# Kernel tuning notes

Measured on AMD Instinct MI355X. Metric: run time of the kernel, lower is better.

The kernel has to match this reference:

```python
import jax, jax.numpy as jnp
import numpy as np

LAMBDA_CHAMFER = 1.0
LAMBDA_EDGE = 0.1


def setup_inputs() -> dict:
    key = jax.random.key(0)
    k1, k2, k3 = jax.random.split(key, 3)
    B, N, M, E = 8, 4096, 4096, 12288
    pred_vertices = jax.random.normal(k1, (B, N, 3), dtype=jnp.float32)
    gt_vertices = jax.random.normal(k2, (B, M, 3), dtype=jnp.float32)
    edges = jax.random.randint(k3, (E, 2), 0, N, dtype=jnp.int64)
    return {"pred_vertices": pred_vertices, "gt_vertices": gt_vertices, "edges": edges}


def _pairwise_dist(p1, p2):
    # ||x - y|| computed via the expanded form to avoid a [B,N,M,3] intermediate.
    # dist2[b,n,m] = |p1[b,n]|^2 + |p2[b,m]|^2 - 2 * p1[b,n] . p2[b,m]
    sq1 = jnp.sum(p1 * p1, axis=-1)  # [B, N]
    sq2 = jnp.sum(p2 * p2, axis=-1)  # [B, M]
    cross = jnp.einsum('bnd,bmd->bnm', p1, p2)  # [B, N, M]
    dist2 = sq1[:, :, None] + sq2[:, None, :] - 2.0 * cross
    return jnp.sqrt(jnp.maximum(dist2, 0.0))


def chamfer_distance(p1, p2):
    dist = _pairwise_dist(p1, p2)  # [B, N, M]
    min_p1 = jnp.min(dist, axis=2)  # [B, N] nearest gt for each pred point
    min_p2 = jnp.min(dist, axis=1)  # [B, M] nearest pred for each gt point
    return jnp.mean(min_p1) + jnp.mean(min_p2)


def edge_length_regularization(vertices, edges):
    v1 = vertices[:, edges[:, 0]]  # [B, E, 3]
    v2 = vertices[:, edges[:, 1]]  # [B, E, 3]
    lengths = jnp.linalg.norm(v1 - v2, axis=2)  # [B, E]
    return jnp.var(lengths, ddof=1)  # torch.var is unbiased by default


def reference(pred_vertices, gt_vertices, edges):
    cd = chamfer_distance(pred_vertices, gt_vertices)
    edge_loss = edge_length_regularization(pred_vertices, edges)
    return LAMBDA_CHAMFER * cd + LAMBDA_EDGE * edge_loss
```

## Files before the change

kernel.cpp:

```cpp
#include <hip/hip_runtime.h>
#include <hip/hip_bf16.h>
#include <float.h>

constexpr int B = 8, N = 4096, M = 4096, E = 12288;
constexpr int TB = 512;
constexpr int EDGE_BLOCKS = (B * E) / TB;
constexpr int QB = 256;
constexpr int CHAM_BLOCKS = 2 * B * (N / QB);
constexpr int SPLIT = 32;
constexpr int RPT = M / SPLIT;
constexpr int VEC = 16;
constexpr int SEGSTRIDE = RPT + 1;
constexpr int REDSTRIDE = QB + 4;


__global__ __launch_bounds__(TB, 4) void fused_kernel(
    const float* __restrict__ pred, const float* __restrict__ gt,
    const int* __restrict__ edges, float* __restrict__ ws) {
    const int bid = blockIdx.x;
    const int t = threadIdx.x;

    __shared__ float4 tile[SPLIT * SEGSTRIDE];
    __shared__ float wsum[8], wsum2[8];
    float* red = (float*)tile;

    if (bid >= EDGE_BLOCKS) {
        const int cb  = bid - EDGE_BLOCKS;
        const int dir = cb >> 7;
        const int b   = (cb >> 4) & 7;
        const int qt  = cb & 15;
        const float* __restrict__ q   = dir ? gt   : pred;
        const float* __restrict__ ref = dir ? pred : gt;

        {
            const float* rb = ref + (size_t)b * M * 3;
#pragma unroll
            for (int r = 0; r < M / TB; ++r) {
                const int g = t + TB * r;
                const float x = rb[3 * g], y = rb[3 * g + 1], z = rb[3 * g + 2];
                tile[(g >> 7) * SEGSTRIDE + (g & 127)] =
                    make_float4(x, y, z, 0.5f * (x * x + y * y + z * z));
            }
        }

        const int qloc = t & 15;
        const int s    = t >> 4;
        float2 nqx2[8], nqy2[8], nqz2[8];
#pragma unroll
        for (int j = 0; j < 8; ++j) {
            const int n0 = qt * QB + qloc + (2 * j) * 16;
            const float* q0 = q + ((size_t)b * N + n0) * 3;
            const float* q1 = q0 + 48;
            nqx2[j] = make_float2(-q0[0], -q1[0]);
            nqy2[j] = make_float2(-q0[1], -q1[1]);
            nqz2[j] = make_float2(-q0[2], -q1[2]);
        }
        __syncthreads();

        const float4* tl = tile + s * SEGSTRIDE;
        float mn[VEC];
#pragma unroll
        for (int i = 0; i < VEC; i++) mn[i] = FLT_MAX;

#pragma unroll 2
        for (int m = 0; m < RPT; m += 2) {
            const float4 a  = tl[m];
            const float4 bb = tl[m + 1];
            const float2 axy = make_float2(a.x, a.y),  azw = make_float2(a.z, a.w);
            const float2 bxy = make_float2(bb.x, bb.y), bzw = make_float2(bb.z, bb.w);
#pragma unroll
            for (int j = 0; j < 8; ++j) {
                float2 ta, tc;
                asm("v_pk_fma_f32 %0, %1, %2, %1 op_sel:[0,0,1] op_sel_hi:[0,1,1]"
                    : "=v"(ta) : "v"(azw), "v"(nqz2[j]));
                asm("v_pk_fma_f32 %0, %1, %2, %0 op_sel:[1,0,0] op_sel_hi:[1,1,1]"
                    : "+v"(ta) : "v"(axy), "v"(nqy2[j]));
                asm("v_pk_fma_f32 %0, %1, %2, %0 op_sel:[0,0,0] op_sel_hi:[0,1,1]"
                    : "+v"(ta) : "v"(axy), "v"(nqx2[j]));
                asm("v_pk_fma_f32 %0, %1, %2, %1 op_sel:[0,0,1] op_sel_hi:[0,1,1]"
                    : "=v"(tc) : "v"(bzw), "v"(nqz2[j]));
                asm("v_pk_fma_f32 %0, %1, %2, %0 op_sel:[1,0,0] op_sel_hi:[1,1,1]"
                    : "+v"(tc) : "v"(bxy), "v"(nqy2[j]));
                asm("v_pk_fma_f32 %0, %1, %2, %0 op_sel:[0,0,0] op_sel_hi:[0,1,1]"
                    : "+v"(tc) : "v"(bxy), "v"(nqx2[j]));
                asm("v_min3_f32 %0, %0, %1, %2"
                    : "+v"(mn[2 * j])     : "v"(ta.x), "v"(tc.x));
                asm("v_min3_f32 %0, %0, %1, %2"
                    : "+v"(mn[2 * j + 1]) : "v"(ta.y), "v"(tc.y));
            }
        }
        __syncthreads();

#pragma unroll
        for (int i = 0; i < VEC; i++)
            red[s * REDSTRIDE + qloc + i * 16] = mn[i];
        __syncthreads();

        float sv = 0.0f;
        if (t < QB) {
            float m = red[t];
#pragma unroll 8
            for (int k = 1; k < SPLIT; k++) m = fminf(m, red[k * REDSTRIDE + t]);
            const float* qp = q + ((size_t)b * N + qt * QB + t) * 3;
            const float sq = qp[0] * qp[0] + qp[1] * qp[1] + qp[2] * qp[2];
            sv = sqrtf(fmaxf(2.0f * m + sq, 0.0f));
        }
#pragma unroll
        for (int o = 32; o > 0; o >>= 1) sv += __shfl_down(sv, o, 64);
        if ((t & 63) == 0) wsum[t >> 6] = sv;
        __syncthreads();
        if (t == 0)
            ws[2 * EDGE_BLOCKS + cb] = wsum[0] + wsum[1] + wsum[2] + wsum[3];
    } else {
        const int eg = bid * TB + t;
        const int b  = eg / E;
        const int e  = eg - b * E;
        const int i0 = edges[2 * e], i1 = edges[2 * e + 1];
        const float* p0 = pred + ((size_t)b * N + i0) * 3;
        const float* p1 = pred + ((size_t)b * N + i1) * 3;
        const float dx = p0[0] - p1[0];
        const float dy = p0[1] - p1[1];
        const float dz = p0[2] - p1[2];
        float L  = sqrtf(dx * dx + dy * dy + dz * dz);
        float L2 = L * L;
#pragma unroll
        for (int o = 32; o > 0; o >>= 1) {
            L  += __shfl_down(L, o, 64);
            L2 += __shfl_down(L2, o, 64);
        }
        const int wv = t >> 6;
        if ((t & 63) == 0) { wsum[wv] = L; wsum2[wv] = L2; }
        __syncthreads();
        if (t == 0) {
            float a = 0.0f, c = 0.0f;
#pragma unroll
            for (int w = 0; w < 8; w++) { a += wsum[w]; c += wsum2[w]; }
            ws[2 * bid]     = a;
            ws[2 * bid + 1] = c;
        }
    }
}

__global__ __launch_bounds__(256) void final_kernel(
    const float* __restrict__ ws, float* __restrict__ out) {
    const int t = threadIdx.x;
    float sc = ws[2 * EDGE_BLOCKS + t];
    float s1 = 0.0f, s2 = 0.0f;
    if (t < EDGE_BLOCKS) {
        s1 = ws[2 * t];
        s2 = ws[2 * t + 1];
    }
#pragma unroll
    for (int o = 32; o > 0; o >>= 1) {
        sc += __shfl_down(sc, o, 64);
        s1 += __shfl_down(s1, o, 64);
        s2 += __shfl_down(s2, o, 64);
    }
    __shared__ float w[3][4];
    const int wv = t >> 6, ln = t & 63;
    if (ln == 0) { w[0][wv] = sc; w[1][wv] = s1; w[2][wv] = s2; }
    __syncthreads();
    if (t == 0) {
        float S = 0.0f, A = 0.0f, C = 0.0f;
#pragma unroll
        for (int i = 0; i < 4; i++) { S += w[0][i]; A += w[1][i]; C += w[2][i]; }
        const float K = (float)(B * E);
        const float var = (C - A * A / K) / (K - 1.0f);
        out[0] = S / 32768.0f + 0.1f * var;
    }
}

extern "C" void kernel_launch(void* const* d_in, const int* in_sizes, int n_in,
                              void* d_out, int out_size, void* d_ws, size_t ws_size,
                              hipStream_t stream) {
    const float* pred  = (const float*)d_in[0];
    const float* gt    = (const float*)d_in[1];
    const int*   edges = (const int*)d_in[2];
    float* out = (float*)d_out;
    float* wsf = (float*)d_ws;

    fused_kernel<<<EDGE_BLOCKS + CHAM_BLOCKS, TB, 0, stream>>>(pred, gt, edges, wsf);
    final_kernel<<<1, 256, 0, stream>>>(wsf, out);
}
```

Baseline: 82.21 us.

## Compute chamfer distances with split-bf16 MFMA and a single bidirectional sweep

New measurement: 86.20 us. 4.9% more time.

```diff
diff --git a/kernel.cpp b/kernel.cpp
--- a/kernel.cpp
+++ b/kernel.cpp
@@ -5,112 +5,135 @@
 constexpr int B = 8, N = 4096, M = 4096, E = 12288;
 constexpr int TB = 512;
 constexpr int EDGE_BLOCKS = (B * E) / TB;
-constexpr int QB = 256;
-constexpr int CHAM_BLOCKS = 2 * B * (N / QB);
-constexpr int SPLIT = 32;
-constexpr int RPT = M / SPLIT;
-constexpr int VEC = 16;
-constexpr int SEGSTRIDE = RPT + 1;
-constexpr int REDSTRIDE = QB + 4;
-
-
-__global__ __launch_bounds__(TB, 4) void fused_kernel(
-    const float* __restrict__ pred, const float* __restrict__ gt,
-    const int* __restrict__ edges, float* __restrict__ ws) {
+constexpr int SWEEP_BLOCKS = B * 16 * 2;
+constexpr size_t BFRAG = 0;
+constexpr size_t ROWP  = 262144;
+constexpr size_t COLP  = 327680;
+constexpr size_t EOFF  = 851968;
+constexpr size_t SUMS  = 852352;
+
+typedef short bf16x8  __attribute__((ext_vector_type(8)));
+typedef float f32x16  __attribute__((ext_vector_type(16)));
+
+__device__ __forceinline__ unsigned short f2bf(float x) {
+    unsigned u = __float_as_uint(x);
+    unsigned r = u + 0x7FFFu + ((u >> 16) & 1u);
+    return (unsigned short)(r >> 16);
+}
+__device__ __forceinline__ float bf2f(unsigned short h) {
+    return __uint_as_float(((unsigned)h) << 16);
+}
+constexpr unsigned short BF_ONE = 0x3F80;
+
+__global__ __launch_bounds__(256) void pack_kernel(
+    const float* __restrict__ gt, unsigned short* __restrict__ bfrag) {
+    const int i = blockIdx.x * 256 + threadIdx.x;
+    const float* p = gt + (size_t)i * 3;
+    const float x = p[0], y = p[1], z = p[2];
+    const unsigned short hx = f2bf(x), hy = f2bf(y), hz = f2bf(z);
+    const float fx = bf2f(hx), fy = bf2f(hy), fz = bf2f(hz);
+    const unsigned short lx = f2bf(x - fx), ly = f2bf(y - fy), lz = f2bf(z - fz);
+    const float c = x * x + y * y + z * z;
+    const unsigned short ch = f2bf(c);
+    const unsigned short cl = f2bf(c - bf2f(ch));
+    const unsigned short ax = f2bf(-2.f * fx), bx = f2bf(-2.f * bf2f(lx));
+    const unsigned short ay = f2bf(-2.f * fy), by = f2bf(-2.f * bf2f(ly));
+    const unsigned short az = f2bf(-2.f * fz), bz = f2bf(-2.f * bf2f(lz));
+
+    unsigned short* d0 = bfrag + (size_t)(((i >> 5) * 64) + (i & 31)) * 8;
+    unsigned short* d1 = d0 + 32 * 8;
+    d0[0] = ax; d0[1] = ax; d0[2] = bx; d0[3] = bx;
+    d0[4] = ay; d0[5] = ay; d0[6] = by; d0[7] = by;
+    d1[0] = az; d1[1] = az; d1[2] = bz; d1[3] = bz;
+    d1[4] = ch; d1[5] = cl; d1[6] = BF_ONE; d1[7] = BF_ONE;
+}
+
+__global__ __launch_bounds__(TB) void sweep_kernel(
+    const float* __restrict__ pred, const unsigned short* __restrict__ bfrag,
+    const int* __restrict__ edges, float* __restrict__ wsf) {
     const int bid = blockIdx.x;
     const int t = threadIdx.x;
-
-    __shared__ float4 tile[SPLIT * SEGSTRIDE];
+    __shared__ unsigned colmin[2048];
     __shared__ float wsum[8], wsum2[8];
-    float* red = (float*)tile;
 
     if (bid >= EDGE_BLOCKS) {
-        const int cb  = bid - EDGE_BLOCKS;
-        const int dir = cb >> 7;
-        const int b   = (cb >> 4) & 7;
-        const int qt  = cb & 15;
-        const float* __restrict__ q   = dir ? gt   : pred;
-        const float* __restrict__ ref = dir ? pred : gt;
-
-        {
-            const float* rb = ref + (size_t)b * M * 3;
-#pragma unroll
-            for (int r = 0; r < M / TB; ++r) {
-                const int g = t + TB * r;
-                const float x = rb[3 * g], y = rb[3 * g + 1], z = rb[3 * g + 2];
-                tile[(g >> 7) * SEGSTRIDE + (g & 127)] =
-                    make_float4(x, y, z, 0.5f * (x * x + y * y + z * z));
-            }
-        }
-
-        const int qloc = t & 15;
-        const int s    = t >> 4;
-        float2 nqx2[8], nqy2[8], nqz2[8];
-#pragma unroll
-        for (int j = 0; j < 8; ++j) {
-            const int n0 = qt * QB + qloc + (2 * j) * 16;
-            const float* q0 = q + ((size_t)b * N + n0) * 3;
-            const float* q1 = q0 + 48;
-            nqx2[j] = make_float2(-q0[0], -q1[0]);
-            nqy2[j] = make_float2(-q0[1], -q1[1]);
-            nqz2[j] = make_float2(-q0[2], -q1[2]);
+        const int sb   = bid - EDGE_BLOCKS;
+        const int b    = sb >> 5;
+        const int nblk = (sb & 31) >> 1;
+        const int mh   = sb & 1;
+        const int wv = t >> 6, l = t & 63;
+        const int nt = nblk * 8 + wv;
+
+        for (int i = t; i < 2048; i += TB) colmin[i] = 0xFFFFFFFFu;
+
+        const float* qp = pred + ((size_t)b * N + nt * 32 + (l & 31)) * 3;
+        const float x = qp[0], y = qp[1], z = qp[2];
+        const unsigned short hx = f2bf(x), hy = f2bf(y), hz = f2bf(z);
+        const unsigned short lx = f2bf(x - bf2f(hx));
+        const unsigned short ly = f2bf(y - bf2f(hy));
+        const unsigned short lz = f2bf(z - bf2f(hz));
+        const float d = x * x + y * y + z * z;
+        const unsigned short dh = f2bf(d);
+        const unsigned short dl = f2bf(d - bf2f(dh));
+        bf16x8 af;
+        if (l < 32) {
+            af[0] = (short)hx; af[1] = (short)lx; af[2] = (short)hx; af[3] = (short)lx;
+            af[4] = (short)hy; af[5] = (short)ly; af[6] = (short)hy; af[7] = (short)ly;
+        } else {
+            af[0] = (short)hz; af[1] = (short)lz; af[2] = (short)hz; af[3] = (short)lz;
+            af[4] = (short)BF_ONE; af[5] = (short)BF_ONE; af[6] = (short)dh; af[7] = (short)dl;
         }
         __syncthreads();
 
-        const float4* tl = tile + s * SEGSTRIDE;
-        float mn[VEC];
-#pragma unroll
-        for (int i = 0; i < VEC; i++) mn[i] = FLT_MAX;
-
-#pragma unroll 2
-        for (int m = 0; m < RPT; m += 2) {
-            const float4 a  = tl[m];
-            const float4 bb = tl[m + 1];
-            const float2 axy = make_float2(a.x, a.y),  azw = make_float2(a.z, a.w);
-            const float2 bxy = make_float2(bb.x, bb.y), bzw = make_float2(bb.z, bb.w);
-#pragma unroll
-            for (int j = 0; j < 8; ++j) {
-                float2 ta, tc;
-                asm("v_pk_fma_f32 %0, %1, %2, %1 op_sel:[0,0,1] op_sel_hi:[0,1,1]"
-                    : "=v"(ta) : "v"(azw), "v"(nqz2[j]));
-                asm("v_pk_fma_f32 %0, %1, %2, %0 op_sel:[1,0,0] op_sel_hi:[1,1,1]"
-                    : "+v"(ta) : "v"(axy), "v"(nqy2[j]));
-                asm("v_pk_fma_f32 %0, %1, %2, %0 op_sel:[0,0,0] op_sel_hi:[0,1,1]"
-                    : "+v"(ta) : "v"(axy), "v"(nqx2[j]));
-                asm("v_pk_fma_f32 %0, %1, %2, %1 op_sel:[0,0,1] op_sel_hi:[0,1,1]"
-                    : "=v"(tc) : "v"(bzw), "v"(nqz2[j]));
-                asm("v_pk_fma_f32 %0, %1, %2, %0 op_sel:[1,0,0] op_sel_hi:[1,1,1]"
-                    : "+v"(tc) : "v"(bxy), "v"(nqy2[j]));
-                asm("v_pk_fma_f32 %0, %1, %2, %0 op_sel:[0,0,0] op_sel_hi:[0,1,1]"
-                    : "+v"(tc) : "v"(bxy), "v"(nqx2[j]));
-                asm("v_min3_f32 %0, %0, %1, %2"
-                    : "+v"(mn[2 * j])     : "v"(ta.x), "v"(tc.x));
-                asm("v_min3_f32 %0, %0, %1, %2"
-                    : "+v"(mn[2 * j + 1]) : "v"(ta.y), "v"(tc.y));
-            }
+        const unsigned short* bp =
+            bfrag + ((size_t)((b * 128 + mh * 64) * 64) + l) * 8;
+        float rowacc[16];
+#pragma unroll
+        for (int r = 0; r < 16; ++r) rowacc[r] = FLT_MAX;
+        f32x16 zacc = {};
+
+        bf16x8 bcur = *(const bf16x8*)bp;
+        for (int mt = 0; mt < 64; ++mt) {
+            const int nx = (mt + 1 < 64) ? mt + 1 : 63;
+            bf16x8 bnxt = *(const bf16x8*)(bp + (size_t)nx * 512);
+            f32x16 D = __builtin_amdgcn_mfma_f32_32x32x16_bf16(af, bcur, zacc, 0, 0, 0);
+#pragma unroll
+            for (int r = 0; r < 16; ++r) rowacc[r] = fminf(rowacc[r], D[r]);
+            float t1, t2, t3, t4, t5, u1, u2;
+            asm("v_min3_f32 %0, %1, %2, %3" : "=v"(t1) : "v"(D[0]),  "v"(D[1]),  "v"(D[2]));
+            asm("v_min3_f32 %0, %1, %2, %3" : "=v"(t2) : "v"(D[3]),  "v"(D[4]),  "v"(D[5]));
+            asm("v_min3_f32 %0, %1, %2, %3" : "=v"(t3) : "v"(D[6]),  "v"(D[7]),  "v"(D[8]));
+            asm("v_min3_f32 %0, %1, %2, %3" : "=v"(t4) : "v"(D[9]),  "v"(D[10]), "v"(D[11]));
+            asm("v_min3_f32 %0, %1, %2, %3" : "=v"(t5) : "v"(D[12]), "v"(D[13]), "v"(D[14]));
+            asm("v_min3_f32 %0, %1, %2, %3" : "=v"(u1) : "v"(t1), "v"(t2), "v"(t3));
+            asm("v_min3_f32 %0, %1, %2, %3" : "=v"(u2) : "v"(t4), "v"(t5), "v"(D[15]));
+            float colv = fminf(u1, u2);
+            colv = fminf(colv, __shfl_xor(colv, 32, 64));
+            atomicMin(&colmin[mt * 32 + (l & 31)], __float_as_uint(fmaxf(colv, 0.f)));
+            bcur = bnxt;
+        }
+
+#pragma unroll
+        for (int r = 0; r < 16; ++r) {
+            float v = rowacc[r];
+            v = fminf(v, __shfl_xor(v, 1, 64));
+            v = fminf(v, __shfl_xor(v, 2, 64));
+            v = fminf(v, __shfl_xor(v, 4, 64));
+            v = fminf(v, __shfl_xor(v, 8, 64));
+            v = fminf(v, __shfl_xor(v, 16, 64));
+            rowacc[r] = v;
+        }
+        if ((l & 31) == 0) {
+            float* rp = wsf + ROWP + ((size_t)(b * 2 + mh) * 128 + nt) * 32;
+            const int hb = (l >> 5) * 4;
+#pragma unroll
+            for (int r = 0; r < 16; ++r)
+                rp[(r & 3) + 8 * (r >> 2) + hb] = fmaxf(rowacc[r], 0.f);
         }
         __syncthreads();
-
-#pragma unroll
-        for (int i = 0; i < VEC; i++)
-            red[s * REDSTRIDE + qloc + i * 16] = mn[i];
-        __syncthreads();
-
-        float sv = 0.0f;
-        if (t < QB) {
-            float m = red[t];
-#pragma unroll 8
-            for (int k = 1; k < SPLIT; k++) m = fminf(m, red[k * REDSTRIDE + t]);
-            const float* qp = q + ((size_t)b * N + qt * QB + t) * 3;
-            const float sq = qp[0] * qp[0] + qp[1] * qp[1] + qp[2] * qp[2];
-            sv = sqrtf(fmaxf(2.0f * m + sq, 0.0f));
-        }
-#pragma unroll
-        for (int o = 32; o > 0; o >>= 1) sv += __shfl_down(sv, o, 64);
-        if ((t & 63) == 0) wsum[t >> 6] = sv;
-        __syncthreads();
-        if (t == 0)
-            ws[2 * EDGE_BLOCKS + cb] = wsum[0] + wsum[1] + wsum[2] + wsum[3];
+        float* cp = wsf + COLP + (size_t)((b * 2 + mh) * 16 + nblk) * 2048;
+        for (int i = t; i < 2048; i += TB)
+            cp[i] = __uint_as_float(colmin[i]);
     } else {
         const int eg = bid * TB + t;
         const int b  = eg / E;
@@ -135,20 +158,46 @@
             float a = 0.0f, c = 0.0f;
 #pragma unroll
             for (int w = 0; w < 8; w++) { a += wsum[w]; c += wsum2[w]; }
-            ws[2 * bid]     = a;
-            ws[2 * bid + 1] = c;
-        }
-    }
-}
-
-__global__ __launch_bounds__(256) void final_kernel(
-    const float* __restrict__ ws, float* __restrict__ out) {
+            wsf[EOFF + 2 * bid]     = a;
+            wsf[EOFF + 2 * bid + 1] = c;
+        }
+    }
+}
+
+__global__ __launch_bounds__(512) void final1_kernel(
+    const float* __restrict__ wsf, float* __restrict__ sums) {
+    const int g = blockIdx.x * 512 + threadIdx.x;
+    const int b = g >> 12, i = g & 4095;
+    const int mh = i >> 11, ci = i & 2047;
+    const float* cp = wsf + COLP + (size_t)((b * 2 + mh) * 16) * 2048 + ci;
+    float cm = cp[0];
+#pragma unroll
+    for (int k = 1; k < 16; ++k) cm = fminf(cm, cp[(size_t)k * 2048]);
+    const float* rp = wsf + ROWP + (size_t)b * 2 * 4096 + i;
+    const float rm = fminf(rp[0], rp[4096]);
+    float sv = sqrtf(cm) + sqrtf(rm);
+#pragma unroll
+    for (int o = 32; o > 0; o >>= 1) sv += __shfl_down(sv, o, 64);
+    __shared__ float w[8];
+    if ((threadIdx.x & 63) == 0) w[threadIdx.x >> 6] = sv;
+    __syncthreads();
+    if (threadIdx.x == 0) {
+        float s = 0.f;
+#pragma unroll
+        for (int k = 0; k < 8; ++k) s += w[k];
+        sums[blockIdx.x] = s;
+    }
+}
+
+__global__ __launch_bounds__(256) void final2_kernel(
+    const float* __restrict__ wsf, const float* __restrict__ sums,
+    float* __restrict__ out) {
     const int t = threadIdx.x;
-    float sc = ws[2 * EDGE_BLOCKS + t];
-    float s1 = 0.0f, s2 = 0.0f;
+    float sc = (t < 64) ? sums[t] : 0.f;
+    float s1 = 0.f, s2 = 0.f;
     if (t < EDGE_BLOCKS) {
-        s1 = ws[2 * t];
-        s2 = ws[2 * t + 1];
+        s1 = wsf[EOFF + 2 * t];
+        s2 = wsf[EOFF + 2 * t + 1];
     }
 #pragma unroll
     for (int o = 32; o > 0; o >>= 1) {
@@ -161,7 +210,7 @@
     if (ln == 0) { w[0][wv] = sc; w[1][wv] = s1; w[2][wv] = s2; }
     __syncthreads();
     if (t == 0) {
-        float S = 0.0f, A = 0.0f, C = 0.0f;
+        float S = 0.f, A = 0.f, C = 0.f;
 #pragma unroll
         for (int i = 0; i < 4; i++) { S += w[0][i]; A += w[1][i]; C += w[2][i]; }
         const float K = (float)(B * E);
@@ -178,7 +227,11 @@
     const int*   edges = (const int*)d_in[2];
     float* out = (float*)d_out;
     float* wsf = (float*)d_ws;
-
-    fused_kernel<<<EDGE_BLOCKS + CHAM_BLOCKS, TB, 0, stream>>>(pred, gt, edges, wsf);
-    final_kernel<<<1, 256, 0, stream>>>(wsf, out);
-}
+    unsigned short* bfrag = (unsigned short*)d_ws;
+    float* sums = wsf + SUMS;
+
+    pack_kernel<<<(B * M) / 256, 256, 0, stream>>>(gt, bfrag);
+    sweep_kernel<<<EDGE_BLOCKS + SWEEP_BLOCKS, TB, 0, stream>>>(pred, bfrag, edges, wsf);
+    final1_kernel<<<64, 512, 0, stream>>>(wsf, sums);
+    final2_kernel<<<1, 256, 0, stream>>>(wsf, sums, out);
+}
```
